# Kernel tuning notes

Hardware: AMD Instinct MI355X
Metric: run time of the kernel (lower is better)

## Reference

```python
import jax, jax.numpy as jnp
import numpy as np

# MORRConfig_20um_MQ ring parameters
A = 0.8578   # attenuation factor a
R = 0.8985   # coupling factor r

IN_C, OUT_C, KS, STRIDE, PAD, MB = 32, 64, 3, 1, 1, 8
WIN = IN_C * KS * KS                      # 288 = kernel_size^2 * in_channel
WIN_PAD = ((WIN + MB - 1) // MB) * MB     # padded to multiple of miniblock
OUT_PAD = ((OUT_C + MB - 1) // MB) * MB
Q = WIN_PAD // MB                         # grid_dim_x = 36
P = OUT_PAD // MB                         # grid_dim_y = 8
MORR_GAIN = (100.0 / (WIN // MB)) ** 0.5  # input power normalization


def mrr_tr(phi):
    # all-pass MORR roundtrip-phase -> transmission intensity
    # T = (a^2 - 2ar cos(phi) + r^2) / (1 - 2ar cos(phi) + (ar)^2)
    c = 2.0 * A * R * jnp.cos(phi)
    return (A * A + R * R - c) / (1.0 + (A * R) ** 2 - c)


def im2col(x):
    # torch F.unfold ordering: feature dim ordered (C, ki, kj)
    B, C, H, W = x.shape
    xp = jnp.pad(x, ((0, 0), (0, 0), (PAD, PAD), (PAD, PAD)))
    Ho = (H + 2 * PAD - KS) // STRIDE + 1
    Wo = (W + 2 * PAD - KS) // STRIDE + 1
    cols = [xp[:, :, i:i + Ho * STRIDE:STRIDE, j:j + Wo * STRIDE:STRIDE]
            for i in range(KS) for j in range(KS)]
    p = jnp.stack(cols, axis=2)               # [B, C, KS*KS, Ho, Wo]
    return p.reshape(B, C * KS * KS, Ho * Wo), Ho, Wo


def setup_inputs() -> dict:
    key = jax.random.key(0)
    k1, k2, k3 = jax.random.split(key, 3)
    x = jax.random.uniform(k1, (8, IN_C, 64, 64), dtype=jnp.float32)  # intensity-encoded, nonneg
    weight = jax.random.uniform(k2, (P, Q, MB), dtype=jnp.float32) * 0.2  # nonneg MORR weights
    morr_output_scale = jax.random.normal(k3, (max(1, Q // 2) + 1,), dtype=jnp.float32) * 0.1
    return {"x": x, "weight": weight, "morr_output_scale": morr_output_scale}


def reference(x, weight, morr_output_scale):
    B = x.shape[0]
    cols, Ho, Wo = im2col(x)
    xb = cols.transpose(0, 2, 1)
    if WIN_PAD > WIN:
        xb = jnp.pad(xb, ((0, 0), (0, 0), (0, WIN_PAD - WIN)))
    xb = xb.reshape(-1, Q, MB)                # [Bs, Q, MB]
    inten = (xb * xb) * MORR_GAIN             # optical intensity (power-normalized)

    # block-circulant weighted phase accumulation == circular conv per (p,q) block, via rFFT
    Wf = jnp.fft.rfft(weight, axis=-1)        # [P, Q, MBf]
    Xf = jnp.fft.rfft(inten, axis=-1)         # [Bs, Q, MBf]
    phase = jnp.fft.irfft(Xf[:, None, :, :] * Wf[None], n=MB, axis=-1)  # [Bs, P, Q, MB]

    tr = mrr_tr(phase)                        # MORR nonlinear transfer

    # differential rails: learnable balancing factor per block-column pair (+1 pad scale)
    half = morr_output_scale[:-1]             # [Q//2]
    if Q % 2 == 0:
        scale = jnp.concatenate([half, -half])                              # [Q]
    else:
        scale = jnp.concatenate([half, morr_output_scale[-1:], -half])      # [Q]

    out = jnp.einsum("bpqk,q->bpk", tr, scale).reshape(-1, OUT_PAD)[:, :OUT_C]
    out = out.reshape(B, Ho * Wo, OUT_C).transpose(0, 2, 1).reshape(B, OUT_C, Ho, Wo)
    return out
```

## Files before the change

### kernel.cpp

```cpp
#include <hip/hip_runtime.h>

#define THREADS 512

#define IN_C 32
#define HW 64
#define Q_N 36

typedef float f32x4 __attribute__((ext_vector_type(4)));
typedef short s16x8 __attribute__((ext_vector_type(8)));

#define AIM_OFF 0
#define WB_OFF  37888
#define ZB_OFF  74752
#define SC_OFF  75264
#define LDS_BYTES 75424

__device__ __forceinline__ unsigned short f2bf(float f) {
    union { float f; unsigned int u; } v; v.f = f;
    unsigned int t = v.u + 0x7FFFu + ((v.u >> 16) & 1u);
    return (unsigned short)(t >> 16);
}

__global__ __launch_bounds__(THREADS, 4)
void morr_conv_kernel(const float* __restrict__ x,
                      const float* __restrict__ weight,
                      const float* __restrict__ mos,
                      float* __restrict__ out)
{
    __shared__ __align__(16) unsigned char lds[LDS_BYTES];
    unsigned short* Aim = (unsigned short*)(lds + AIM_OFF);
    unsigned short* Wb  = (unsigned short*)(lds + WB_OFF);
    float* scl          = (float*)(lds + SC_OFF);

    const int tid = threadIdx.x;
    const int blk = blockIdx.x;
    const int b   = blk >> 6;
    const int row = blk & 63;

    const float GI = 1.6666666666666667f * 0.15915494309189535f;
    const float A_ = 0.8578f, R_ = 0.8985f;
    const float S_ = A_ * A_ + R_ * R_;
    const float D_ = 1.f + (A_ * R_) * (A_ * R_);
    const float C2 = 2.f * A_ * R_;
    const float E_ = S_ - D_;

    {
        const int px = tid & 63;
        const int g  = tid >> 6;
#pragma unroll
        for (int c2 = 0; c2 < 4; ++c2) {
            const int c = g * 4 + c2;
            const float* xc = x + ((b * IN_C + c) * HW) * HW;
#pragma unroll
            for (int ki = 0; ki < 3; ++ki) {
                const int gh = row + ki - 1;
                const bool rok = (unsigned)gh < 64u;
#pragma unroll
                for (int kj = 0; kj < 3; ++kj) {
                    const int gw = px + kj - 1;
                    float v = (rok && (unsigned)gw < 64u) ? xc[gh * HW + gw] : 0.f;
                    Aim[px * 296 + c * 9 + ki * 3 + kj] = f2bf(GI * v * v);
                }
            }
        }
    }
#pragma unroll
    for (int i = 0; i < 36; ++i) {
        const int idx = tid + 512 * i;
        const int q  = idx >> 9;
        const int mt = (idx >> 7) & 3;
        const int pr = (idx >> 3) & 15;
        const int j  = idx & 7;
        const int pk = mt * 16 + pr;
        const int p  = pk >> 3, k = pk & 7;
        Wb[idx] = f2bf(weight[p * 288 + q * 8 + ((k - j) & 7)]);
    }
    if (tid < 256) ((unsigned short*)(lds + ZB_OFF))[tid] = 0;
    if (tid < Q_N) scl[tid] = ((tid < 18) ? mos[tid] : -mos[tid - 18]) * E_;
    __syncthreads();

    const int wv = tid >> 6;
    const int l  = tid & 63;
    const int ll = l & 15;
    const int lh = l >> 4;
    const int nt = wv & 3;
    const int m0 = (wv >> 2) * 2;

    const unsigned short* bB = Aim + (nt * 16 + ll) * 296;
    const unsigned short* aW = (l < 16)
        ? (Wb + (m0 * 16 + ll) * 8)
        : (const unsigned short*)(lds + ZB_OFF);
    const int qstep = (l < 16) ? 512 : 0;

    float acc[8];
#pragma unroll
    for (int i = 0; i < 8; ++i) acc[i] = 0.f;

    const f32x4 cz = {0.f, 0.f, 0.f, 0.f};

#pragma unroll
    for (int q = 0; q < Q_N; ++q) {
        s16x8 bfrag = *(const s16x8*)(bB + q * 8);
        s16x8 a0 = *(const s16x8*)(aW);
        s16x8 a1 = *(const s16x8*)(aW + 128);
        f32x4 d0 = __builtin_amdgcn_mfma_f32_16x16x32_bf16(a0, bfrag, cz, 0, 0, 0);
        f32x4 d1 = __builtin_amdgcn_mfma_f32_16x16x32_bf16(a1, bfrag, cz, 0, 0, 0);
        const float sc = scl[q];
#pragma unroll
        for (int r = 0; r < 4; ++r) {
            float c0 = __builtin_amdgcn_cosf(d0[r]);
            acc[r]     = fmaf(sc, __builtin_amdgcn_rcpf(fmaf(-C2, c0, D_)), acc[r]);
            float c1 = __builtin_amdgcn_cosf(d1[r]);
            acc[4 + r] = fmaf(sc, __builtin_amdgcn_rcpf(fmaf(-C2, c1, D_)), acc[4 + r]);
        }
        aW += qstep;
    }

    const int col = nt * 16 + ll;
#pragma unroll
    for (int t = 0; t < 2; ++t) {
#pragma unroll
        for (int r = 0; r < 4; ++r) {
            const int pk = (m0 + t) * 16 + lh * 4 + r;
            out[(b * 64 + pk) * (HW * HW) + row * HW + col] = acc[t * 4 + r];
        }
    }
}

extern "C" void kernel_launch(void* const* d_in, const int* in_sizes, int n_in,
                              void* d_out, int out_size, void* d_ws, size_t ws_size,
                              hipStream_t stream) {
    const float* x      = (const float*)d_in[0];
    const float* weight = (const float*)d_in[1];
    const float* mos    = (const float*)d_in[2];
    float* out = (float*)d_out;

    dim3 grid(512), block(THREADS);
    hipLaunchKernelGGL(morr_conv_kernel, grid, block, 0, stream, x, weight, mos, out);
}
```

Baseline: 86.06 us.

## Split preprocessing into separate kernel, stream bf16 intensities and weights from workspace

Adds a pre-pass kernel that squares, scales and converts x to bf16 once per element and builds the expanded circulant weight matrix and scales in global workspace. The main kernel then gathers 2-byte values instead of recomputing conversions nine times per element, and reads weight fragments and scales directly from global memory instead of staging them in LDS, which cuts LDS use and may raise occupancy. The cost is a second launch, an extra global round-trip for the converted input, and weight loads from L2 inside the MFMA loop.

```diff
diff --git a/kernel.cpp b/kernel.cpp
--- a/kernel.cpp
+++ b/kernel.cpp
@@ -1,6 +1,4 @@
 #include <hip/hip_runtime.h>
-
-#define THREADS 512
 
 #define IN_C 32
 #define HW 64
@@ -8,12 +6,12 @@
 
 typedef float f32x4 __attribute__((ext_vector_type(4)));
 typedef short s16x8 __attribute__((ext_vector_type(8)));
+typedef short s16x4 __attribute__((ext_vector_type(4)));
 
-#define AIM_OFF 0
-#define WB_OFF  37888
-#define ZB_OFF  74752
-#define SC_OFF  75264
-#define LDS_BYTES 75424
+#define WEXP_OFF 0
+#define ZW_OFF   73728
+#define SCL_OFF  74240
+#define GX2_OFF  75776
 
 __device__ __forceinline__ unsigned short f2bf(float f) {
     union { float f; unsigned int u; } v; v.f = f;
@@ -21,36 +19,72 @@
     return (unsigned short)(t >> 16);
 }
 
-__global__ __launch_bounds__(THREADS, 4)
-void morr_conv_kernel(const float* __restrict__ x,
-                      const float* __restrict__ weight,
-                      const float* __restrict__ mos,
+#define A_C 0.8578f
+#define R_C 0.8985f
+#define S_C (A_C*A_C + R_C*R_C)
+#define D_C (1.f + (A_C*R_C)*(A_C*R_C))
+#define C2_C (2.f*A_C*R_C)
+#define E_C (S_C - D_C)
+#define GI_C (1.6666666666666667f * 0.15915494309189535f)
+
+__global__ __launch_bounds__(512)
+void morr_pre(const float* __restrict__ x,
+              const float* __restrict__ weight,
+              const float* __restrict__ mos,
+              unsigned char* __restrict__ ws)
+{
+    const int tid = threadIdx.x;
+    const int blk = blockIdx.x;
+    if (blk < 512) {
+        const int i = (blk * 512 + tid) * 4;
+        float4 v = *(const float4*)(x + i);
+        unsigned short o0 = f2bf(GI_C * v.x * v.x);
+        unsigned short o1 = f2bf(GI_C * v.y * v.y);
+        unsigned short o2 = f2bf(GI_C * v.z * v.z);
+        unsigned short o3 = f2bf(GI_C * v.w * v.w);
+        s16x4 o = {(short)o0, (short)o1, (short)o2, (short)o3};
+        *(s16x4*)(ws + GX2_OFF + (size_t)i * 2) = o;
+    } else {
+        unsigned short* wexp = (unsigned short*)(ws + WEXP_OFF);
+#pragma unroll
+        for (int it = 0; it < 72; ++it) {
+            const int idx = tid + 512 * it;
+            const int q  = idx >> 9;
+            const int mt = (idx >> 7) & 3;
+            const int pr = (idx >> 3) & 15;
+            const int j  = idx & 7;
+            const int pk = mt * 16 + pr;
+            const int p  = pk >> 3, k = pk & 7;
+            wexp[idx] = f2bf(weight[p * 288 + q * 8 + ((k - j) & 7)]);
+        }
+        if (tid < 128) ((float*)(ws + ZW_OFF))[tid] = 0.f;
+        if (tid < Q_N)
+            ((float*)(ws + SCL_OFF))[tid] =
+                ((tid < 18) ? mos[tid] : -mos[tid - 18]) * E_C;
+    }
+}
+
+__global__ __launch_bounds__(512, 4)
+void morr_conv_kernel(const unsigned char* __restrict__ ws,
                       float* __restrict__ out)
 {
-    __shared__ __align__(16) unsigned char lds[LDS_BYTES];
-    unsigned short* Aim = (unsigned short*)(lds + AIM_OFF);
-    unsigned short* Wb  = (unsigned short*)(lds + WB_OFF);
-    float* scl          = (float*)(lds + SC_OFF);
+    __shared__ __align__(16) unsigned short Aim[64 * 296];
 
     const int tid = threadIdx.x;
     const int blk = blockIdx.x;
     const int b   = blk >> 6;
     const int row = blk & 63;
 
-    const float GI = 1.6666666666666667f * 0.15915494309189535f;
-    const float A_ = 0.8578f, R_ = 0.8985f;
-    const float S_ = A_ * A_ + R_ * R_;
-    const float D_ = 1.f + (A_ * R_) * (A_ * R_);
-    const float C2 = 2.f * A_ * R_;
-    const float E_ = S_ - D_;
+    const unsigned short* gx2 = (const unsigned short*)(ws + GX2_OFF);
 
     {
         const int px = tid & 63;
         const int g  = tid >> 6;
+        unsigned short buf[36];
 #pragma unroll
-        for (int c2 = 0; c2 < 4; ++c2) {
-            const int c = g * 4 + c2;
-            const float* xc = x + ((b * IN_C + c) * HW) * HW;
+        for (int cc = 0; cc < 4; ++cc) {
+            const int c = g * 4 + cc;
+            const unsigned short* xc = gx2 + ((b * IN_C + c) << 12);
 #pragma unroll
             for (int ki = 0; ki < 3; ++ki) {
                 const int gh = row + ki - 1;
@@ -58,25 +92,20 @@
 #pragma unroll
                 for (int kj = 0; kj < 3; ++kj) {
                     const int gw = px + kj - 1;
-                    float v = (rok && (unsigned)gw < 64u) ? xc[gh * HW + gw] : 0.f;
-                    Aim[px * 296 + c * 9 + ki * 3 + kj] = f2bf(GI * v * v);
+                    unsigned short v = 0;
+                    if (rok && (unsigned)gw < 64u) v = xc[(gh << 6) + gw];
+                    buf[cc * 9 + ki * 3 + kj] = v;
                 }
             }
         }
+        unsigned short* dst = Aim + px * 296 + g * 36;
+#pragma unroll
+        for (int i = 0; i < 9; ++i) {
+            s16x4 v = {(short)buf[i*4], (short)buf[i*4+1],
+                       (short)buf[i*4+2], (short)buf[i*4+3]};
+            *(s16x4*)(dst + i * 4) = v;
+        }
     }
-#pragma unroll
-    for (int i = 0; i < 36; ++i) {
-        const int idx = tid + 512 * i;
-        const int q  = idx >> 9;
-        const int mt = (idx >> 7) & 3;
-        const int pr = (idx >> 3) & 15;
-        const int j  = idx & 7;
-        const int pk = mt * 16 + pr;
-        const int p  = pk >> 3, k = pk & 7;
-        Wb[idx] = f2bf(weight[p * 288 + q * 8 + ((k - j) & 7)]);
-    }
-    if (tid < 256) ((unsigned short*)(lds + ZB_OFF))[tid] = 0;
-    if (tid < Q_N) scl[tid] = ((tid < 18) ? mos[tid] : -mos[tid - 18]) * E_;
     __syncthreads();
 
     const int wv = tid >> 6;
@@ -87,10 +116,11 @@
     const int m0 = (wv >> 2) * 2;
 
     const unsigned short* bB = Aim + (nt * 16 + ll) * 296;
-    const unsigned short* aW = (l < 16)
-        ? (Wb + (m0 * 16 + ll) * 8)
-        : (const unsigned short*)(lds + ZB_OFF);
-    const int qstep = (l < 16) ? 512 : 0;
+    const unsigned short* aW;
+    int qs;
+    if (l < 16) { aW = (const unsigned short*)(ws + WEXP_OFF) + (m0 * 16 + ll) * 8; qs = 512; }
+    else        { aW = (const unsigned short*)(ws + ZW_OFF);                        qs = 0;   }
+    const float* __restrict__ sp = (const float*)(ws + SCL_OFF);
 
     float acc[8];
 #pragma unroll
@@ -101,19 +131,18 @@
 #pragma unroll
     for (int q = 0; q < Q_N; ++q) {
         s16x8 bfrag = *(const s16x8*)(bB + q * 8);
-        s16x8 a0 = *(const s16x8*)(aW);
-        s16x8 a1 = *(const s16x8*)(aW + 128);
+        s16x8 a0 = *(const s16x8*)(aW + q * qs);
+        s16x8 a1 = *(const s16x8*)(aW + q * qs + 128);
         f32x4 d0 = __builtin_amdgcn_mfma_f32_16x16x32_bf16(a0, bfrag, cz, 0, 0, 0);
         f32x4 d1 = __builtin_amdgcn_mfma_f32_16x16x32_bf16(a1, bfrag, cz, 0, 0, 0);
-        const float sc = scl[q];
+        const float sc = sp[q];
 #pragma unroll
         for (int r = 0; r < 4; ++r) {
             float c0 = __builtin_amdgcn_cosf(d0[r]);
-            acc[r]     = fmaf(sc, __builtin_amdgcn_rcpf(fmaf(-C2, c0, D_)), acc[r]);
+            acc[r]     = fmaf(sc, __builtin_amdgcn_rcpf(fmaf(-C2_C, c0, D_C)), acc[r]);
             float c1 = __builtin_amdgcn_cosf(d1[r]);
-            acc[4 + r] = fmaf(sc, __builtin_amdgcn_rcpf(fmaf(-C2, c1, D_)), acc[4 + r]);
+            acc[4 + r] = fmaf(sc, __builtin_amdgcn_rcpf(fmaf(-C2_C, c1, D_C)), acc[4 + r]);
         }
-        aW += qstep;
     }
 
     const int col = nt * 16 + ll;
@@ -134,7 +163,8 @@
     const float* weight = (const float*)d_in[1];
     const float* mos    = (const float*)d_in[2];
     float* out = (float*)d_out;
+    unsigned char* ws = (unsigned char*)d_ws;
 
-    dim3 grid(512), block(THREADS);
-    hipLaunchKernelGGL(morr_conv_kernel, grid, block, 0, stream, x, weight, mos, out);
+    hipLaunchKernelGGL(morr_pre, dim3(513), dim3(512), 0, stream, x, weight, mos, ws);
+    hipLaunchKernelGGL(morr_conv_kernel, dim3(512), dim3(512), 0, stream, ws, out);
 }
```

After: 83.50 us. 1.03x faster.
